# Performance work log

Hardware: AMD Instinct MI355X
Metric: run time of the kernel (lower is better)

## Reference

```python
import jax, jax.numpy as jnp
import numpy as np

TEXT_VOCAB = 32000
CB = 1024          # audio_codebook_size
NCB = 8            # audio_num_codebooks
H = 2048           # hidden_size
NH = 16            # attention heads
NKV = 4            # kv heads (GQA)
HD = H // NH       # head dim = 128
FF = 8192          # ffn intermediate
L = 2              # num layers
EPS = 1e-5


def rmsnorm(x, w):
    v = jnp.mean(x * x, axis=-1, keepdims=True)
    return x * jax.lax.rsqrt(v + EPS) * w


def rope(x, pos):
    # x: [B,S,h,d], rotate-half style RoPE
    d = x.shape[-1]
    inv = 1.0 / (10000.0 ** (jnp.arange(0, d, 2, dtype=jnp.float32) / d))
    ang = pos[:, None] * inv[None, :]                 # [S, d/2]
    cos = jnp.cos(ang)[None, :, None, :]
    sin = jnp.sin(ang)[None, :, None, :]
    x1, x2 = x[..., : d // 2], x[..., d // 2 :]
    return jnp.concatenate([x1 * cos - x2 * sin, x2 * cos + x1 * sin], axis=-1)


def attention(x, wq, wk, wv, wo, pos, mask_bias):
    B, S, _ = x.shape
    q = (x @ wq).reshape(B, S, NH, HD)
    k = (x @ wk).reshape(B, S, NKV, HD)
    v = (x @ wv).reshape(B, S, NKV, HD)
    q = rope(q, pos)
    k = rope(k, pos)
    k = jnp.repeat(k, NH // NKV, axis=2)
    v = jnp.repeat(v, NH // NKV, axis=2)
    scores = jnp.einsum('bqhd,bkhd->bhqk', q, k) / np.float32(np.sqrt(HD))
    p = jax.nn.softmax(scores + mask_bias, axis=-1)
    o = jnp.einsum('bhqk,bkhd->bqhd', p, v).reshape(B, S, NH * HD)
    return o @ wo


def mlp(x, wfc, wproj):
    return jax.nn.silu(x @ wfc) @ wproj


def setup_inputs() -> dict:
    key = jax.random.key(0)
    ks = jax.random.split(key, 20)
    s = 0.02
    inp = {
        'input_ids': jax.random.randint(ks[0], (1, 2048), 0, TEXT_VOCAB + CB, dtype=jnp.int64 if jax.config.jax_enable_x64 else jnp.int32),
        'vocab_emb': jax.random.normal(ks[1], (TEXT_VOCAB, H), jnp.float32) * s,
        'audio_emb': jax.random.normal(ks[2], (NCB * CB, H), jnp.float32) * s,
        'ln_in_text': jnp.ones((L, H), jnp.float32),
        'ln_in_audio': jnp.ones((L, H), jnp.float32),
        'ln_post_text': jnp.ones((L, H), jnp.float32),
        'ln_post_audio': jnp.ones((L, H), jnp.float32),
        'wq': jax.random.normal(ks[3], (L, H, NH * HD), jnp.float32) * s,
        'wk': jax.random.normal(ks[4], (L, H, NKV * HD), jnp.float32) * s,
        'wv': jax.random.normal(ks[5], (L, H, NKV * HD), jnp.float32) * s,
        'wo': jax.random.normal(ks[6], (L, NH * HD, H), jnp.float32) * s,
        'wfc_text': jax.random.normal(ks[7], (L, H, FF), jnp.float32) * s,
        'wproj_text': jax.random.normal(ks[8], (L, FF, H), jnp.float32) * s,
        'wfc_audio': jax.random.normal(ks[9], (L, H, FF), jnp.float32) * s,
        'wproj_audio': jax.random.normal(ks[10], (L, FF, H), jnp.float32) * s,
        'ln_f': jnp.ones((H,), jnp.float32),
    }
    return inp


def reference(input_ids, vocab_emb, audio_emb, ln_in_text, ln_in_audio,
              ln_post_text, ln_post_audio, wq, wk, wv, wo,
              wfc_text, wproj_text, wfc_audio, wproj_audio, ln_f):
    B, S = input_ids.shape
    amask = input_ids > TEXT_VOCAB - 1                      # [B,S] audio-token mask
    text_tok = jnp.where(amask, TEXT_VOCAB - 1, input_ids)
    text_e = vocab_emb[text_tok]                            # [B,S,H]
    audio_tok = jnp.where(amask, input_ids - TEXT_VOCAB, 0)
    shift = (jnp.arange(NCB) * CB)[:, None, None]           # [NCB,1,1]
    audio_e = audio_emb[audio_tok[None] + shift].sum(0)     # sum over codebooks -> [B,S,H]
    h = jnp.where(amask[..., None], audio_e, text_e)

    pos = jnp.arange(S, dtype=jnp.float32)
    causal = jnp.tril(jnp.ones((S, S), bool))
    mask_bias = jnp.where(causal, 0.0, -1e9).astype(jnp.float32)[None, None]
    m = amask[..., None]

    for i in range(L):
        res = h
        hn = jnp.where(m, rmsnorm(h, ln_in_audio[i]), rmsnorm(h, ln_in_text[i]))
        h = res + attention(hn, wq[i], wk[i], wv[i], wo[i], pos, mask_bias)
        res = h
        t = mlp(rmsnorm(h, ln_post_text[i]), wfc_text[i], wproj_text[i])
        a = mlp(rmsnorm(h, ln_post_audio[i]), wfc_audio[i], wproj_audio[i])
        h = res + jnp.where(m, a, t)

    return rmsnorm(h, ln_f)
```

## Files before the change

kernel.cpp:

```cpp
#include <hip/hip_runtime.h>
#include <hip/hip_bf16.h>
#include <math.h>

#define S_LEN 2048
#define HID   2048

typedef __bf16 bf16x8 __attribute__((ext_vector_type(8)));
typedef float  f32x4  __attribute__((ext_vector_type(4)));

__device__ __forceinline__ unsigned short f2b(float x) {
  __hip_bfloat16 h = __float2bfloat16(x);
  return __builtin_bit_cast(unsigned short, h);
}

__device__ __forceinline__ float block_sum_256(float v) {
  __shared__ float red[4];
  #pragma unroll
  for (int o = 32; o > 0; o >>= 1) v += __shfl_down(v, o, 64);
  if ((threadIdx.x & 63) == 0) red[threadIdx.x >> 6] = v;
  __syncthreads();
  v = red[0] + red[1] + red[2] + red[3];
  __syncthreads();
  return v;
}

__global__ __launch_bounds__(256) void embed_kernel(
    const int* __restrict__ ids, const float* __restrict__ vemb,
    const float* __restrict__ aemb, float* __restrict__ h, int* __restrict__ amask) {
  const int s = blockIdx.x;
  const int id = ids[s];
  const bool am = id > 31999;
  if (threadIdx.x == 0) amask[s] = am ? 1 : 0;
  const int d0 = threadIdx.x * 8;
  float out[8];
  if (am) {
    const int at = id - 32000;
    #pragma unroll
    for (int u = 0; u < 8; u++) out[u] = 0.f;
    for (int cb = 0; cb < 8; cb++) {
      const float* src = aemb + (long)(at + cb * 1024) * HID + d0;
      #pragma unroll
      for (int u = 0; u < 8; u++) out[u] += src[u];
    }
  } else {
    const float* src = vemb + (long)id * HID + d0;
    #pragma unroll
    for (int u = 0; u < 8; u++) out[u] = src[u];
  }
  float* dst = h + (long)s * HID + d0;
  #pragma unroll
  for (int u = 0; u < 8; u++) dst[u] = out[u];
}

__global__ __launch_bounds__(256) void partition_rows(
    const int* __restrict__ ids, int* __restrict__ apos, int* __restrict__ cnt) {
  __shared__ int ca[256];
  __shared__ int sc[257];
  const int t = threadIdx.x;
  int m[8], loc = 0;
  #pragma unroll
  for (int i = 0; i < 8; i++) { m[i] = ids[t * 8 + i] > 31999 ? 1 : 0; loc += m[i]; }
  ca[t] = loc;
  __syncthreads();
  if (t == 0) {
    int run = 0;
    for (int i = 0; i < 256; i++) { sc[i] = run; run += ca[i]; }
    sc[256] = run;
  }
  __syncthreads();
  int off = sc[t];
  #pragma unroll
  for (int i = 0; i < 8; i++) {
    const int s = t * 8 + i;
    if (m[i]) { apos[s] = off; off++; }
    else apos[s] = -1;
  }
  if (t == 0) { cnt[0] = sc[256]; cnt[1] = (sc[256] + 127) & ~127; }
}

__global__ __launch_bounds__(256) void init_stats(
    float* __restrict__ stm, float* __restrict__ stl, int* __restrict__ ctrs) {
  const int i = blockIdx.x * 256 + threadIdx.x;
  stm[i] = -1e30f;
  stl[i] = 0.f;
  if (i < 4) ctrs[i] = 0;
}

__global__ __launch_bounds__(256) void transposew(
    const float* __restrict__ W, int ldw, unsigned short* __restrict__ Wt, int K, int N,
    long srcZ, long dstZ) {
  W += (long)blockIdx.z * srcZ;
  Wt += (long)blockIdx.z * dstZ;
  __shared__ float t[64][65];
  const int k0 = blockIdx.y * 64, n0 = blockIdx.x * 64;
  const int q = threadIdx.x & 15;
  const int r0 = threadIdx.x >> 4;
  #pragma unroll
  for (int i = 0; i < 4; i++) {
    const int row = r0 + i * 16;
    const float4 v = *(const float4*)(W + (long)(k0 + row) * ldw + n0 + q * 4);
    t[row][q * 4 + 0] = v.x; t[row][q * 4 + 1] = v.y;
    t[row][q * 4 + 2] = v.z; t[row][q * 4 + 3] = v.w;
  }
  __syncthreads();
  #pragma unroll
  for (int i = 0; i < 4; i++) {
    const int n = r0 + i * 16;
    ushort4 o;
    o.x = f2b(t[q * 4 + 0][n]); o.y = f2b(t[q * 4 + 1][n]);
    o.z = f2b(t[q * 4 + 2][n]); o.w = f2b(t[q * 4 + 3][n]);
    *(ushort4*)(Wt + (long)(n0 + n) * K + k0 + q * 4) = o;
  }
}

__global__ __launch_bounds__(256) void transpose_b16(
    const unsigned short* __restrict__ V, unsigned short* __restrict__ Vt) {
  __shared__ unsigned short t[64][72];
  const int s0 = blockIdx.y * 64, d0 = blockIdx.x * 64;
  const int q = threadIdx.x & 15;
  const int r0 = threadIdx.x >> 4;
  #pragma unroll
  for (int i = 0; i < 4; i++) {
    const int row = r0 + i * 16;
    const ushort4 v = *(const ushort4*)(V + (long)(s0 + row) * 512 + d0 + q * 4);
    t[row][q * 4 + 0] = v.x; t[row][q * 4 + 1] = v.y;
    t[row][q * 4 + 2] = v.z; t[row][q * 4 + 3] = v.w;
  }
  __syncthreads();
  #pragma unroll
  for (int i = 0; i < 4; i++) {
    const int d = r0 + i * 16;
    ushort4 o;
    o.x = t[q * 4 + 0][d]; o.y = t[q * 4 + 1][d];
    o.z = t[q * 4 + 2][d]; o.w = t[q * 4 + 3][d];
    *(ushort4*)(Vt + (long)(d0 + d) * 2048 + s0 + q * 4) = o;
  }
}

__global__ __launch_bounds__(256) void rope_table(float* __restrict__ c, float* __restrict__ s_) {
  const int i = blockIdx.x * 256 + threadIdx.x;
  const int pos = i >> 6, j = i & 63;
  const float inv = powf(10000.f, -(float)(2 * j) * (1.f / 128.f));
  const float ang = (float)pos * inv;
  c[i] = cosf(ang);
  s_[i] = sinf(ang);
}

__global__ __launch_bounds__(256) void rmsnorm_sel(
    const float* __restrict__ x, const int* __restrict__ amask,
    const float* __restrict__ wt, const float* __restrict__ wa, unsigned short* __restrict__ out) {
  const long s = blockIdx.x;
  const float* xr = x + s * HID;
  const int d0 = threadIdx.x * 8;
  float v[8], ss = 0.f;
  #pragma unroll
  for (int u = 0; u < 8; u++) { v[u] = xr[d0 + u]; ss += v[u] * v[u]; }
  ss = block_sum_256(ss) * (1.f / HID);
  const float rr = rsqrtf(ss + 1e-5f);
  const float* w = amask[s] ? wa : wt;
  #pragma unroll
  for (int u = 0; u < 8; u++) out[s * HID + d0 + u] = f2b(v[u] * rr * w[d0 + u]);
}

__global__ __launch_bounds__(256) void rmsnorm_post(
    const float* __restrict__ x, const int* __restrict__ apos,
    const float* __restrict__ wt, const float* __restrict__ wa,
    unsigned short* __restrict__ hnt, unsigned short* __restrict__ hna_g) {
  const long s = blockIdx.x;
  const float* xr = x + s * HID;
  const int d0 = threadIdx.x * 8;
  float v[8], ss = 0.f;
  #pragma unroll
  for (int u = 0; u < 8; u++) { v[u] = xr[d0 + u]; ss += v[u] * v[u]; }
  ss = block_sum_256(ss) * (1.f / HID);
  const float rr = rsqrtf(ss + 1e-5f);
  const int ap = apos[s];
  #pragma unroll
  for (int u = 0; u < 8; u++) {
    const float xn = v[u] * rr;
    hnt[s * HID + d0 + u] = f2b(xn * wt[d0 + u]);
    if (ap >= 0) hna_g[(long)ap * HID + d0 + u] = f2b(xn * wa[d0 + u]);
  }
}

__global__ __launch_bounds__(256) void rmsnorm_final(
    const float* __restrict__ x, const float* __restrict__ w, float* __restrict__ out) {
  const long s = blockIdx.x;
  const float* xr = x + s * HID;
  const int d0 = threadIdx.x * 8;
  float v[8], ss = 0.f;
  #pragma unroll
  for (int u = 0; u < 8; u++) { v[u] = xr[d0 + u]; ss += v[u] * v[u]; }
  ss = block_sum_256(ss) * (1.f / HID);
  const float rr = rsqrtf(ss + 1e-5f);
  #pragma unroll
  for (int u = 0; u < 8; u++) out[s * HID + d0 + u] = v[u] * rr * w[d0 + u];
}

__device__ __forceinline__ void gload16(const void* g, void* l) {
  __builtin_amdgcn_global_load_lds((const __attribute__((address_space(1))) void*)g,
                                   (__attribute__((address_space(3))) void*)l, 16, 0, 0);
}

#define ABAR() do { __builtin_amdgcn_s_barrier(); \
  asm volatile("" ::: "memory"); __builtin_amdgcn_sched_barrier(0); } while (0)

__global__ __launch_bounds__(512, 1) void attn_flash(
    const unsigned short* __restrict__ qb, const unsigned short* __restrict__ kb,
    const unsigned short* __restrict__ vt, float* __restrict__ opart,
    float* __restrict__ stm, float* __restrict__ stl,
    int* __restrict__ ctr, float iscale) {
  __shared__ __align__(16) unsigned short Kb[2][2][128][64];
  __shared__ __align__(16) unsigned short Vb[2][128][64];
  __shared__ __align__(16) unsigned short Pb[8][16][144];
  __shared__ int s_item;
  const int tid = threadIdx.x;
  const int lane = tid & 63;
  const int w = tid >> 6;
  const int lr = lane & 15;
  const int kg = lane >> 4;
  const int trow = tid >> 3;
  const int tc = tid & 7;

  for (;;) {
    if (tid == 0) s_item = atomicAdd(ctr, 1);
    __syncthreads();
    const int item = s_item;
    __syncthreads();
    if (item >= 512) break;
    const int qq = 15 - (item >> 5);
    const int h = item & 15;
    const int cch = (item >> 4) & 1;
    const int kvh = h >> 2;
    const int bm = qq * 128;
    const int nt = qq + 1;
    const int tmid = (nt + 1) >> 1;
    const int t0 = cch ? tmid : 0;
    const int t1 = cch ? nt : tmid;
    if (t0 >= t1) continue;

    bf16x8 af_q[4];
    {
      const unsigned short* qr = qb + (long)(bm + w * 16 + lr) * 2048 + h * 128 + kg * 8;
      #pragma unroll
      for (int c = 0; c < 4; c++) af_q[c] = *(const bf16x8*)(qr + c * 32);
    }
    float m[4], l[4];
    #pragma unroll
    for (int r = 0; r < 4; r++) { m[r] = -1e30f; l[r] = 0.f; }
    f32x4 acc_o[8];
    #pragma unroll
    for (int nf = 0; nf < 8; nf++) acc_o[nf] = (f32x4){0.f, 0.f, 0.f, 0.f};

    auto stageK = [&](int buf, int t) {
      const int kv0 = t * 128;
      #pragma unroll
      for (int hh2 = 0; hh2 < 2; hh2++)
        #pragma unroll
        for (int rr = 0; rr < 2; rr++) {
          const int row = trow + rr * 64;
          gload16(kb + (long)(kv0 + row) * 512 + kvh * 128 + hh2 * 64 + ((tc ^ (row & 7)) * 8),
                  &Kb[buf][hh2][row][tc * 8]);
        }
    };
    auto stageV = [&](int t) {
      const int kv0 = t * 128;
      #pragma unroll
      for (int hh2 = 0; hh2 < 2; hh2++)
        #pragma unroll
        for (int rr = 0; rr < 2; rr++) {
          const int row = trow + rr * 64;
          gload16(vt + (long)(kvh * 128 + row) * 2048 + kv0 + hh2 * 64 + ((tc ^ (row & 7)) * 8),
                  &Vb[hh2][row][tc * 8]);
        }
    };

    stageK(t0 & 1, t0);
    for (int t = t0; t < t1; t++) {
      const bool hn = (t + 1) < t1;
      stageV(t);
      if (hn) stageK((t + 1) & 1, t + 1);
      if (hn) { asm volatile("s_waitcnt vmcnt(8)" ::: "memory"); }
      else    { asm volatile("s_waitcnt vmcnt(4)" ::: "memory"); }
      ABAR();
      f32x4 acc[8];
      #pragma unroll
      for (int nf = 0; nf < 8; nf++) acc[nf] = (f32x4){0.f, 0.f, 0.f, 0.f};
      #pragma unroll
      for (int c = 0; c < 4; c++) {
        #pragma unroll
        for (int nf = 0; nf < 8; nf++) {
          const int row = nf * 16 + lr;
          bf16x8 bk = *(const bf16x8*)(&Kb[t & 1][c >> 1][row][(((c & 1) * 4 + kg) ^ (row & 7)) * 8]);
          acc[nf] = __builtin_amdgcn_mfma_f32_16x16x32_bf16(af_q[c], bk, acc[nf], 0, 0, 0);
        }
      }
      const bool diag = (t == nt - 1);
      #pragma unroll
      for (int r = 0; r < 4; r++) {
        const int rowg = bm + w * 16 + kg * 4 + r;
        float sv[8], tmax = -1e30f;
        #pragma unroll
        for (int nf = 0; nf < 8; nf++) {
          float s = acc[nf][r] * iscale;
          const int colg = t * 128 + nf * 16 + lr;
          if (diag && colg > rowg) s = -1e30f;
          sv[nf] = s;
          tmax = fmaxf(tmax, s);
        }
        #pragma unroll
        for (int o = 1; o < 16; o <<= 1) tmax = fmaxf(tmax, __shfl_xor(tmax, o, 64));
        const float mn = fmaxf(m[r], tmax);
        const float scal = __expf(m[r] - mn);
        float psum = 0.f;
        #pragma unroll
        for (int nf = 0; nf < 8; nf++) {
          const float pe = __expf(sv[nf] - mn);
          psum += pe;
          Pb[w][kg * 4 + r][nf * 16 + lr] = f2b(pe);
        }
        #pragma unroll
        for (int o = 1; o < 16; o <<= 1) psum += __shfl_xor(psum, o, 64);
        l[r] = l[r] * scal + psum;
        m[r] = mn;
        #pragma unroll
        for (int nf = 0; nf < 8; nf++) acc_o[nf][r] *= scal;
      }
      asm volatile("s_waitcnt lgkmcnt(0)" ::: "memory");
      __builtin_amdgcn_sched_barrier(0);
      if (hn) { asm volatile("s_waitcnt vmcnt(4)" ::: "memory"); }
      else    { asm volatile("s_waitcnt vmcnt(0)" ::: "memory"); }
      ABAR();
      #pragma unroll
      for (int c = 0; c < 4; c++) {
        bf16x8 ap = *(const bf16x8*)(&Pb[w][lr][c * 32 + kg * 8]);
        #pragma unroll
        for (int nf = 0; nf < 8; nf++) {
          const int row = nf * 16 + lr;
          bf16x8 bv = *(const bf16x8*)(&Vb[c >> 1][row][(((c & 1) * 4 + kg) ^ (row & 7)) * 8]);
          acc_o[nf] = __builtin_amdgcn_mfma_f32_16x16x32_bf16(ap, bv, acc_o[nf], 0, 0, 0);
        }
      }
      ABAR();
    }
    float* op = opart + (long)cch * 4194304;
    #pragma unroll
    for (int nf = 0; nf < 8; nf++)
      #pragma unroll
      for (int r = 0; r < 4; r++)
        op[(long)(bm + w * 16 + kg * 4 + r) * 2048 + h * 128 + nf * 16 + lr] = acc_o[nf][r];
    if (lr == 0) {
      #pragma unroll
      for (int r = 0; r < 4; r++) {
        const int row = bm + w * 16 + kg * 4 + r;
        stm[(cch * 16 + h) * 2048 + row] = m[r];
        stl[(cch * 16 + h) * 2048 + row] = l[r];
      }
    }
    __syncthreads();
  }
}

__global__ __launch_bounds__(256) void o_merge2(
    const float* __restrict__ op, const float* __restrict__ stm,
    const float* __restrict__ stl, unsigned short* __restrict__ o) {
  const int i = blockIdx.x * 256 + threadIdx.x;
  const int s = i >> 11, c = i & 2047, h = c >> 7;
  const int si = h * 2048 + s;
  const float m1 = stm[si], l1 = stl[si];
  const float m2 = stm[32768 + si], l2 = stl[32768 + si];
  const float M = fmaxf(m1, m2);
  const float w1 = __expf(m1 - M), w2 = __expf(m2 - M);
  const float denom = l1 * w1 + l2 * w2;
  o[i] = f2b((op[i] * w1 + op[i + 4194304] * w2) / denom);
}

__global__ __launch_bounds__(256) void mlp_reduce(
    const float* __restrict__ pt, const float* __restrict__ pa,
    const int* __restrict__ apos, float* __restrict__ h) {
  const int i = blockIdx.x * 256 + threadIdx.x;
  const int r = i >> 11, c = i & 2047;
  const long Z = (long)1 << 22;
  const int ap = apos[r];
  float val;
  if (ap < 0) {
    val = pt[i] + pt[i + Z] + pt[i + 2 * Z] + pt[i + 3 * Z];
  } else {
    const long b = (long)ap * 2048 + c;
    val = 0.f;
    #pragma unroll
    for (int k = 0; k < 8; k++) val += pa[k * Z + b];
  }
  h[i] += val;
}

__device__ __forceinline__ void xcd_swizzle(int& bx, int& by, int& bz) {
  const int gx = gridDim.x, gy = gridDim.y;
  const long nwg = (long)gx * gy * gridDim.z;
  const long lin = blockIdx.x + (long)gx * (blockIdx.y + (long)gy * blockIdx.z);
  const long cpx = nwg >> 3;
  const long w = (lin & 7) * cpx + (lin >> 3);
  bx = (int)(w % gx);
  const long t = w / gx;
  by = (int)(t % gy);
  bz = (int)(t / gy);
}

template <int BM, int BN, int EPI, int SWZ>
__global__ __launch_bounds__(512) void gemm2(
    const unsigned short* __restrict__ A, int lda, long sAz,
    const unsigned short* __restrict__ Bt, int ldb, long sBz,
    void* __restrict__ Cv, int ldc, long sCz, long sCx, int K, float scale,
    const int* __restrict__ ecnt, int kspl,
    const float* __restrict__ rc, const float* __restrict__ rs,
    unsigned short* __restrict__ kbo, unsigned short* __restrict__ vbo) {
  constexpr int MF = BM / 32;
  constexpr int NF = BN / 64;
  __shared__ __align__(16) unsigned short smem[2 * (BM + BN) * 64];
  const int tid = threadIdx.x;
  const int lane = tid & 63;
  const int wave = tid >> 6;
  int bxi = blockIdx.x, byi = blockIdx.y, bzi = blockIdx.z;
  if constexpr (SWZ) xcd_swizzle(bxi, byi, bzi);
  const int bm = byi * BM;
  const int z = bzi;
  int bn, kbeg, nt;
  if constexpr (EPI == 7) {
    bn = bxi * BN;
    kbeg = z * kspl;
    nt = kspl / 64;
  } else {
    bn = bxi * BN;
    kbeg = 0;
    nt = K / 64;
  }
  if constexpr (EPI == 2 || EPI == 7) {
    if (bm >= ecnt[1]) return;
  }
  A += sAz * z;
  Bt += sBz * z;
  const int wm = (wave >> 2) * (BM / 2);
  const int wn = (wave & 3) * (BN / 4);
  const int lr = lane & 15;
  const int kg = lane >> 4;
  const int swx = lr & 7;
  const int trow = tid >> 3;
  const int tc = tid & 7;
  const long aoff = (long)(bm + trow) * lda + ((tc ^ (trow & 7)) * 8);
  const long boff = (long)(bn + trow) * ldb + ((tc ^ (trow & 7)) * 8);

  f32x4 acc[MF][NF];
  #pragma unroll
  for (int m = 0; m < MF; m++)
    #pragma unroll
    for (int n = 0; n < NF; n++) acc[m][n] = (f32x4){0.f, 0.f, 0.f, 0.f};

  auto stage = [&](int buf, int k0) {
    unsigned short* sA = &smem[(size_t)buf * (BM + BN) * 64];
    #pragma unroll
    for (int r = 0; r < BM / 64; r++)
      gload16(A + aoff + (long)r * 64 * lda + k0, sA + r * 4096 + tid * 8);
    unsigned short* sB = sA + BM * 64;
    #pragma unroll
    for (int r = 0; r < BN / 64; r++)
      gload16(Bt + boff + (long)r * 64 * ldb + k0, sB + r * 4096 + tid * 8);
  };
  auto compute = [&](int buf) {
    const unsigned short* sA = &smem[(size_t)buf * (BM + BN) * 64];
    const unsigned short* sB = sA + BM * 64;
    #pragma unroll
    for (int ks = 0; ks < 2; ks++) {
      bf16x8 af[MF], bv[NF];
      #pragma unroll
      for (int m = 0; m < MF; m++) {
        const int row = wm + m * 16 + lr;
        af[m] = *(const bf16x8*)(sA + row * 64 + (((ks * 4 + kg) ^ swx) * 8));
      }
      #pragma unroll
      for (int n = 0; n < NF; n++) {
        const int row = wn + n * 16 + lr;
        bv[n] = *(const bf16x8*)(sB + row * 64 + (((ks * 4 + kg) ^ swx) * 8));
      }
      #pragma unroll
      for (int m = 0; m < MF; m++)
        #pragma unroll
        for (int n = 0; n < NF; n++)
          acc[m][n] = __builtin_amdgcn_mfma_f32_16x16x32_bf16(af[m], bv[n], acc[m][n], 0, 0, 0);
    }
  };

  if (nt > 0) {
    stage(0, kbeg);
    asm volatile("s_waitcnt vmcnt(0)" ::: "memory");
    __syncthreads();
    int cur = 0;
    for (int t = 0; t < nt; t++) {
      if (t + 1 < nt) stage(cur ^ 1, kbeg + (t + 1) * 64);
      compute(cur);
      asm volatile("s_waitcnt vmcnt(0)" ::: "memory");
      __syncthreads();
      cur ^= 1;
    }
  }

  if constexpr (EPI == 8) {
    if (bn >= 2560) {
      #pragma unroll
      for (int m = 0; m < MF; m++)
        #pragma unroll
        for (int n = 0; n < NF; n++)
          #pragma unroll
          for (int r = 0; r < 4; r++) {
            const int grow = bm + wm + m * 16 + kg * 4 + r;
            const int gcol = bn + wn + n * 16 + lr;
            vbo[(long)grow * 512 + (gcol - 2560)] = f2b(acc[m][n][r]);
          }
    } else {
      float* Cl = (float*)smem;
      #pragma unroll
      for (int m = 0; m < MF; m++)
        #pragma unroll
        for (int n = 0; n < NF; n++)
          #pragma unroll
          for (int r = 0; r < 4; r++)
            Cl[(wm + m * 16 + kg * 4 + r) * 128 + wn + n * 16 + lr] = acc[m][n][r];
      __syncthreads();
      const int j = tid & 63;
      const int r2 = tid >> 6;
      #pragma unroll
      for (int it = 0; it < 16; it++) {
        const int row = r2 + it * 8;
        const int s = bm + row;
        const float c = rc[s * 64 + j], sn = rs[s * 64 + j];
        const float x1 = Cl[row * 128 + j], x2 = Cl[row * 128 + j + 64];
        const unsigned short o1 = f2b(x1 * c - x2 * sn);
        const unsigned short o2 = f2b(x2 * c + x1 * sn);
        if (bn < 2048) {
          unsigned short* qp = (unsigned short*)Cv + (long)s * 2048 + bn + j;
          qp[0] = o1; qp[64] = o2;
        } else {
          unsigned short* kp = kbo + (long)s * 512 + (bn - 2048) + j;
          kp[0] = o1; kp[64] = o2;
        }
      }
    }
    return;
  }

  #pragma unroll
  for (int m = 0; m < MF; m++) {
    #pragma unroll
    for (int n = 0; n < NF; n++) {
      #pragma unroll
      for (int r = 0; r < 4; r++) {
        const int grow = bm + wm + m * 16 + kg * 4 + r;
        const int gcol = bn + wn + n * 16 + lr;
        const long idx = (long)grow * ldc + gcol;
        float v = acc[m][n][r];
        if constexpr (EPI == 2) {
          ((unsigned short*)Cv)[idx] = f2b(v / (1.f + expf(-v)));
        } else if constexpr (EPI == 3) {
          ((float*)Cv)[idx] += v;
        } else if constexpr (EPI == 7) {
          ((float*)Cv)[(long)z * sCz + idx] = v;
        }
      }
    }
  }
}

template <int EPI>
__global__ __launch_bounds__(512, 1) void gemm8(
    const unsigned short* __restrict__ A0, const unsigned short* __restrict__ A1, int lda,
    const unsigned short* __restrict__ Bt, long sBz, int ldb,
    void* __restrict__ Cv, int ldc, long sCz, int K) {
  __shared__ __align__(16) unsigned short smem[2][4][8192];
  const int tid = threadIdx.x;
  const int lane = tid & 63;
  const int wave = tid >> 6;
  int bxi = blockIdx.x, byi = blockIdx.y, bzi = blockIdx.z;
  xcd_swizzle(bxi, byi, bzi);
  const int bm = byi * 256;
  const int bn = bxi * 256;
  const int z = bzi;
  const unsigned short* Aq;
  const unsigned short* Bq;
  if constexpr (EPI == 10) {
    Aq = z ? A1 : A0;
    Bq = Bt + (long)z * sBz;
  } else {
    Aq = A0 + z * 2048;
    Bq = Bt + z * 2048;
  }
  const int nt = K / 64;
  const int trow = tid >> 3;
  const int tc = tid & 7;
  const int sws = (tc ^ (trow & 7)) * 8;
  const int lr = lane & 15;
  const int kg = lane >> 4;
  const int wr = (wave >> 2) * 64;
  const int wc = (wave & 3) * 32;

  f32x4 acc[2][2][4][2];
  #pragma unroll
  for (int mh = 0; mh < 2; mh++)
    #pragma unroll
    for (int nh = 0; nh < 2; nh++)
      #pragma unroll
      for (int mf = 0; mf < 4; mf++)
        #pragma unroll
        for (int nf = 0; nf < 2; nf++) acc[mh][nh][mf][nf] = (f32x4){0.f, 0.f, 0.f, 0.f};

  bf16x8 af[2][4], af2[2][4], bv0[2][2], bv1[2][2];

  auto stageA = [&](int buf, int half, int k0) {
    const unsigned short* g = Aq + (long)(bm + half * 128 + trow) * lda + k0 + sws;
    unsigned short* l = &smem[buf][half][0] + tid * 8;
    gload16(g, l);
    gload16(g + (long)64 * lda, l + 4096);
  };
  auto stageB = [&](int buf, int half, int k0) {
    const unsigned short* g = Bq + (long)(bn + half * 128 + trow) * ldb + k0 + sws;
    unsigned short* l = &smem[buf][2 + half][0] + tid * 8;
    gload16(g, l);
    gload16(g + (long)64 * ldb, l + 4096);
  };

#define GSYNC(VM) \
  asm volatile("s_waitcnt vmcnt(" #VM ")" ::: "memory"); \
  __builtin_amdgcn_s_barrier(); \
  asm volatile("" ::: "memory"); \
  __builtin_amdgcn_sched_barrier(0)

#define RD_A(BUF, MH, DST) do { \
    _Pragma("unroll") \
    for (int ks = 0; ks < 2; ++ks) { \
      _Pragma("unroll") \
      for (int mf = 0; mf < 4; ++mf) { \
        const int row = wr + mf * 16 + lr; \
        DST[ks][mf] = *(const bf16x8*)(&smem[BUF][MH][0] + row * 64 + (((ks * 4 + kg) ^ (row & 7)) * 8)); \
      } \
    } \
  } while (0)

#define RD_B(BUF, NH, DST) do { \
    _Pragma("unroll") \
    for (int ks = 0; ks < 2; ++ks) { \
      _Pragma("unroll") \
      for (int nf = 0; nf < 2; ++nf) { \
        const int row = wc + nf * 16 + lr; \
        DST[ks][nf] = *(const bf16x8*)(&smem[BUF][2 + NH][0] + row * 64 + (((ks * 4 + kg) ^ (row & 7)) * 8)); \
      } \
    } \
  } while (0)

#define DO_MFMA(MH, NH, AF, BV) do { \
    __builtin_amdgcn_s_setprio(1); \
    _Pragma("unroll") \
    for (int ks = 0; ks < 2; ++ks) \
      _Pragma("unroll") \
      for (int mf = 0; mf < 4; ++mf) \
        _Pragma("unroll") \
        for (int nf = 0; nf < 2; ++nf) \
          acc[MH][NH][mf][nf] = __builtin_amdgcn_mfma_f32_16x16x32_bf16( \
              AF[ks][mf], BV[ks][nf], acc[MH][NH][mf][nf], 0, 0, 0); \
    __builtin_amdgcn_s_setprio(0); \
  } while (0)

  stageA(0, 0, 0); stageB(0, 0, 0); stageB(0, 1, 0); stageA(0, 1, 0);
  stageA(1, 0, 64); stageB(1, 1, 64); stageB(1, 0, 64);
  GSYNC(8);

  for (int t = 0; t <= nt - 3; ++t) {
    const int b = t & 1, nb = b ^ 1;
    const int k1 = (t + 1) << 6, k2 = (t + 2) << 6;
    RD_A(b, 0, af); RD_B(b, 0, bv0); RD_B(b, 1, bv1);
    stageA(nb, 1, k1); DO_MFMA(0, 0, af, bv0); GSYNC(8);
    RD_A(b, 1, af2);
    stageA(b, 0, k2); DO_MFMA(0, 1, af, bv1); GSYNC(8);
    stageB(b, 1, k2); DO_MFMA(1, 1, af2, bv1); GSYNC(8);
    RD_B(b, 0, bv0);
    stageB(b, 0, k2); DO_MFMA(1, 0, af2, bv0); GSYNC(8);
  }
  {
    const int t = nt - 2;
    const int b = t & 1, nb = b ^ 1;
    const int k1 = (t + 1) << 6;
    RD_A(b, 0, af); RD_B(b, 0, bv0); RD_B(b, 1, bv1);
    stageA(nb, 1, k1); DO_MFMA(0, 0, af, bv0); GSYNC(8);
    RD_A(b, 1, af2); DO_MFMA(0, 1, af, bv1); GSYNC(8);
    DO_MFMA(1, 1, af2, bv1); GSYNC(8);
    RD_B(b, 0, bv0); DO_MFMA(1, 0, af2, bv0); GSYNC(2);
  }
  {
    const int b = (nt - 1) & 1;
    RD_A(b, 0, af); RD_B(b, 0, bv0); RD_B(b, 1, bv1);
    DO_MFMA(0, 0, af, bv0); GSYNC(0);
    RD_A(b, 1, af2); DO_MFMA(0, 1, af, bv1);
    DO_MFMA(1, 1, af2, bv1);
    RD_B(b, 0, bv0); DO_MFMA(1, 0, af2, bv0);
  }
#undef DO_MFMA
#undef RD_B
#undef RD_A
#undef GSYNC

  #pragma unroll
  for (int mh = 0; mh < 2; mh++) {
    #pragma unroll
    for (int nh = 0; nh < 2; nh++) {
      #pragma unroll
      for (int mf = 0; mf < 4; mf++) {
        #pragma unroll
        for (int nf = 0; nf < 2; nf++) {
          #pragma unroll
          for (int r = 0; r < 4; r++) {
            const int grow = bm + mh * 128 + wr + mf * 16 + kg * 4 + r;
            const int gcol = bn + nh * 128 + wc + nf * 16 + lr;
            const long idx = (long)z * sCz + (long)grow * ldc + gcol;
            const float v = acc[mh][nh][mf][nf][r];
            if constexpr (EPI == 10) {
              ((unsigned short*)Cv)[idx] = f2b(v / (1.f + expf(-v)));
            } else {
              ((float*)Cv)[idx] = v;
            }
          }
        }
      }
    }
  }
}

__global__ __launch_bounds__(256) void fill_zero(float* p, long n) {
  const long i = (long)blockIdx.x * 256 + threadIdx.x;
  if (i < n) p[i] = 0.f;
}

extern "C" void kernel_launch(void* const* d_in, const int* in_sizes, int n_in,
                              void* d_out, int out_size, void* d_ws, size_t ws_size,
                              hipStream_t stream) {
  const int* ids = (const int*)d_in[0];
  const float* vocab_emb = (const float*)d_in[1];
  const float* audio_emb = (const float*)d_in[2];
  const float* ln_in_text = (const float*)d_in[3];
  const float* ln_in_audio = (const float*)d_in[4];
  const float* ln_post_text = (const float*)d_in[5];
  const float* ln_post_audio = (const float*)d_in[6];
  const float* wq = (const float*)d_in[7];
  const float* wk = (const float*)d_in[8];
  const float* wv = (const float*)d_in[9];
  const float* wo = (const float*)d_in[10];
  const float* wfc_t = (const float*)d_in[11];
  const float* wpj_t = (const float*)d_in[12];
  const float* wfc_a = (const float*)d_in[13];
  const float* wpj_a = (const float*)d_in[14];
  const float* ln_f = (const float*)d_in[15];

  size_t off = 0;
  auto alloc = [&](size_t bytes) -> void* {
    void* p = (char*)d_ws + off;
    off += (bytes + 255) & ~(size_t)255;
    return p;
  };
  const size_t LW = 77594624;
  unsigned short* wsT = (unsigned short*)alloc((size_t)2 * LW * 2);
  int* amask = (int*)alloc(S_LEN * 4);
  int* apos = (int*)alloc(S_LEN * 4);
  int* cnt = (int*)alloc(16);
  int* ctrs = (int*)alloc(16);
  float* ropec = (float*)alloc((size_t)S_LEN * 64 * 4);
  float* ropes = (float*)alloc((size_t)S_LEN * 64 * 4);
  float* h = (float*)alloc((size_t)S_LEN * HID * 4);
  unsigned short* hn = (unsigned short*)alloc((size_t)S_LEN * HID * 2);
  unsigned short* hnt = (unsigned short*)alloc((size_t)S_LEN * HID * 2);
  unsigned short* hna_g = (unsigned short*)alloc((size_t)S_LEN * HID * 2);
  unsigned short* qb = (unsigned short*)alloc((size_t)S_LEN * 2048 * 2);
  unsigned short* kb = (unsigned short*)alloc((size_t)S_LEN * 512 * 2);
  unsigned short* vb = (unsigned short*)alloc((size_t)S_LEN * 512 * 2);
  unsigned short* vt = (unsigned short*)alloc((size_t)512 * S_LEN * 2);
  unsigned short* o = (unsigned short*)alloc((size_t)S_LEN * 2048 * 2);
  float* stm = (float*)alloc((size_t)2 * 16 * 2048 * 4);
  float* stl = (float*)alloc((size_t)2 * 16 * 2048 * 4);
  char* big = (char*)alloc(268435456);
  float* opart = (float*)big;
  unsigned short* mlp_t = (unsigned short*)big;
  unsigned short* mlp_a = (unsigned short*)(big + 33554432);
  float* pt = (float*)(big + 67108864);
  float* pa = (float*)(big + 134217728);

  if (ws_size < off) {
    fill_zero<<<(out_size + 255) / 256, 256, 0, stream>>>((float*)d_out, out_size);
    return;
  }

  const size_t WO_ = 6291456, WFT = 10485760, WPT = 27262976, WFA = 44040192, WPA = 60817408;

  embed_kernel<<<S_LEN, 256, 0, stream>>>(ids, vocab_emb, audio_emb, h, amask);
  partition_rows<<<1, 256, 0, stream>>>(ids, apos, cnt);
  init_stats<<<256, 256, 0, stream>>>(stm, stl, ctrs);
  rope_table<<<S_LEN * 64 / 256, 256, 0, stream>>>(ropec, ropes);

  const long LWl = (long)LW;
  transposew<<<dim3(32, 32, 2), 256, 0, stream>>>(wq, 2048, wsT, 2048, 2048, 4194304, LWl);
  transposew<<<dim3(8, 32, 2), 256, 0, stream>>>(wk, 512, wsT + 4194304, 2048, 512, 1048576, LWl);
  transposew<<<dim3(8, 32, 2), 256, 0, stream>>>(wv, 512, wsT + 5242880, 2048, 512, 1048576, LWl);
  transposew<<<dim3(32, 32, 2), 256, 0, stream>>>(wo, 2048, wsT + WO_, 2048, 2048, 4194304, LWl);
  transposew<<<dim3(128, 32, 2), 256, 0, stream>>>(wfc_t, 8192, wsT + WFT, 2048, 8192, 16777216, LWl);
  transposew<<<dim3(32, 128, 2), 256, 0, stream>>>(wpj_t, 2048, wsT + WPT, 8192, 2048, 16777216, LWl);
  transposew<<<dim3(128, 32, 2), 256, 0, stream>>>(wfc_a, 8192, wsT + WFA, 2048, 8192, 16777216, LWl);
  transposew<<<dim3(32, 128, 2), 256, 0, stream>>>(wpj_a, 2048, wsT + WPA, 8192, 2048, 16777216, LWl);

  const float iscale = 0.08838834764831845f;
  for (int i = 0; i < 2; i++) {
    const size_t wb = (size_t)i * LW;
    rmsnorm_sel<<<S_LEN, 256, 0, stream>>>(h, amask, ln_in_text + i * HID, ln_in_audio + i * HID, hn);
    gemm2<128, 128, 8, 1><<<dim3(24, 16, 1), 512, 0, stream>>>(hn, 2048, 0, wsT + wb, 2048, 0,
        qb, 2048, 0, 0, 2048, 1.f, nullptr, 0, ropec, ropes, kb, vb);
    transpose_b16<<<dim3(8, 32), 256, 0, stream>>>(vb, vt);
    attn_flash<<<256, 512, 0, stream>>>(qb, kb, vt, opart, stm, stl, ctrs + i, iscale);
    o_merge2<<<16384, 256, 0, stream>>>(opart, stm, stl, o);
    gemm2<128, 128, 3, 1><<<dim3(16, 16, 1), 512, 0, stream>>>(o, 2048, 0, wsT + wb + WO_, 2048, 0,
        h, 2048, 0, 0, 2048, 1.f, nullptr, 0, nullptr, nullptr, nullptr, nullptr);
    rmsnorm_post<<<S_LEN, 256, 0, stream>>>(h, apos, ln_post_text + i * HID, ln_post_audio + i * HID, hnt, hna_g);
    gemm2<128, 128, 2, 0><<<dim3(64, 16, 1), 512, 0, stream>>>(hna_g, 2048, 0, wsT + wb + WFA, 2048, 0,
        mlp_a, 8192, 0, 0, 2048, 1.f, cnt, 0, nullptr, nullptr, nullptr, nullptr);
    gemm8<10><<<dim3(32, 8, 1), 512, 0, stream>>>(hnt, hnt, 2048, wsT + wb + WFT, 0, 2048,
        mlp_t, 8192, 0, 2048);
    gemm2<128, 128, 7, 0><<<dim3(16, 16, 8), 512, 0, stream>>>(mlp_a, 8192, 0, wsT + wb + WPA, 8192, 0,
        pa, 2048, (long)1 << 22, 0, 8192, 1.f, cnt, 1024, nullptr, nullptr, nullptr, nullptr);
    gemm8<11><<<dim3(8, 8, 4), 512, 0, stream>>>(mlp_t, mlp_t, 8192, wsT + wb + WPT, 0, 8192,
        pt, 2048, (long)1 << 22, 2048);
    mlp_reduce<<<16384, 256, 0, stream>>>(pt, pa, apos, h);
  }
  rmsnorm_final<<<S_LEN, 256, 0, stream>>>(h, ln_f, (float*)d_out);
}
```

Before: 968.4 us.

## Fuse MLP reduce with next RMSNorm and split-K the audio fc GEMM

Merges the MLP partial-sum reduction with the following layer's input RMSNorm, or with the final norm on the last layer. This removes a separate rmsnorm pass and an extra read of h. The audio up-projection GEMM now runs split-K with two z-slices writing fp32 partials, and a new silu_reduce kernel sums them and applies SiLU. This adds parallelism for the small audio-row GEMM, at the cost of an extra fp32 write/read pass and a kernel launch.

```diff
diff --git a/kernel.cpp b/kernel.cpp
--- a/kernel.cpp
+++ b/kernel.cpp
@@ -183,18 +183,58 @@
   }
 }
 
-__global__ __launch_bounds__(256) void rmsnorm_final(
-    const float* __restrict__ x, const float* __restrict__ w, float* __restrict__ out) {
+template <int MODE>
+__global__ __launch_bounds__(256) void mlp_reduce_norm(
+    const float* __restrict__ pt, const float* __restrict__ pa,
+    const int* __restrict__ apos, const int* __restrict__ amask,
+    float* __restrict__ h, const float* __restrict__ wt, const float* __restrict__ wa,
+    void* __restrict__ out) {
   const long s = blockIdx.x;
-  const float* xr = x + s * HID;
   const int d0 = threadIdx.x * 8;
-  float v[8], ss = 0.f;
-  #pragma unroll
-  for (int u = 0; u < 8; u++) { v[u] = xr[d0 + u]; ss += v[u] * v[u]; }
+  const long Z = (long)1 << 22;
+  const int ap = apos[s];
+  const long base = s * HID + d0;
+  float hv[8], ss = 0.f;
+  #pragma unroll
+  for (int u = 0; u < 8; u++) {
+    float val;
+    if (ap < 0) {
+      val = pt[base + u] + pt[base + u + Z] + pt[base + u + 2 * Z] + pt[base + u + 3 * Z];
+    } else {
+      const long b = (long)ap * 2048 + d0 + u;
+      val = 0.f;
+      #pragma unroll
+      for (int k = 0; k < 8; k++) val += pa[k * Z + b];
+    }
+    hv[u] = h[base + u] + val;
+    ss += hv[u] * hv[u];
+  }
+  if constexpr (MODE == 0) {
+    #pragma unroll
+    for (int u = 0; u < 8; u++) h[base + u] = hv[u];
+  }
   ss = block_sum_256(ss) * (1.f / HID);
   const float rr = rsqrtf(ss + 1e-5f);
-  #pragma unroll
-  for (int u = 0; u < 8; u++) out[s * HID + d0 + u] = v[u] * rr * w[d0 + u];
+  if constexpr (MODE == 0) {
+    const float* w = amask[s] ? wa : wt;
+    #pragma unroll
+    for (int u = 0; u < 8; u++) ((unsigned short*)out)[base + u] = f2b(hv[u] * rr * w[d0 + u]);
+  } else {
+    #pragma unroll
+    for (int u = 0; u < 8; u++) ((float*)out)[base + u] = hv[u] * rr * wt[d0 + u];
+  }
+}
+
+__global__ __launch_bounds__(256) void silu_reduce(
+    const float* __restrict__ p, const int* __restrict__ cnt, unsigned short* __restrict__ out) {
+  const int i = blockIdx.x * 2048 + threadIdx.x * 8;
+  const int r = i >> 13;
+  if (r >= cnt[1]) return;
+  #pragma unroll
+  for (int u = 0; u < 8; u++) {
+    const float v = p[i + u] + p[i + u + (1 << 24)];
+    out[i + u] = f2b(v / (1.f + expf(-v)));
+  }
 }
 
 __device__ __forceinline__ void gload16(const void* g, void* l) {
@@ -373,25 +413,6 @@
   const float w1 = __expf(m1 - M), w2 = __expf(m2 - M);
   const float denom = l1 * w1 + l2 * w2;
   o[i] = f2b((op[i] * w1 + op[i + 4194304] * w2) / denom);
-}
-
-__global__ __launch_bounds__(256) void mlp_reduce(
-    const float* __restrict__ pt, const float* __restrict__ pa,
-    const int* __restrict__ apos, float* __restrict__ h) {
-  const int i = blockIdx.x * 256 + threadIdx.x;
-  const int r = i >> 11, c = i & 2047;
-  const long Z = (long)1 << 22;
-  const int ap = apos[r];
-  float val;
-  if (ap < 0) {
-    val = pt[i] + pt[i + Z] + pt[i + 2 * Z] + pt[i + 3 * Z];
-  } else {
-    const long b = (long)ap * 2048 + c;
-    val = 0.f;
-    #pragma unroll
-    for (int k = 0; k < 8; k++) val += pa[k * Z + b];
-  }
-  h[i] += val;
 }
 
 __device__ __forceinline__ void xcd_swizzle(int& bx, int& by, int& bz) {
@@ -787,6 +808,7 @@
   unsigned short* mlp_a = (unsigned short*)(big + 33554432);
   float* pt = (float*)(big + 67108864);
   float* pa = (float*)(big + 134217728);
+  float* pfa = (float*)(big + 134217728);
 
   if (ws_size < off) {
     fill_zero<<<(out_size + 255) / 256, 256, 0, stream>>>((float*)d_out, out_size);
@@ -811,9 +833,9 @@
   transposew<<<dim3(32, 128, 2), 256, 0, stream>>>(wpj_a, 2048, wsT + WPA, 8192, 2048, 16777216, LWl);
 
   const float iscale = 0.08838834764831845f;
+  rmsnorm_sel<<<S_LEN, 256, 0, stream>>>(h, amask, ln_in_text, ln_in_audio, hn);
   for (int i = 0; i < 2; i++) {
     const size_t wb = (size_t)i * LW;
-    rmsnorm_sel<<<S_LEN, 256, 0, stream>>>(h, amask, ln_in_text + i * HID, ln_in_audio + i * HID, hn);
     gemm2<128, 128, 8, 1><<<dim3(24, 16, 1), 512, 0, stream>>>(hn, 2048, 0, wsT + wb, 2048, 0,
         qb, 2048, 0, 0, 2048, 1.f, nullptr, 0, ropec, ropes, kb, vb);
     transpose_b16<<<dim3(8, 32), 256, 0, stream>>>(vb, vt);
@@ -822,15 +844,21 @@
     gemm2<128, 128, 3, 1><<<dim3(16, 16, 1), 512, 0, stream>>>(o, 2048, 0, wsT + wb + WO_, 2048, 0,
         h, 2048, 0, 0, 2048, 1.f, nullptr, 0, nullptr, nullptr, nullptr, nullptr);
     rmsnorm_post<<<S_LEN, 256, 0, stream>>>(h, apos, ln_post_text + i * HID, ln_post_audio + i * HID, hnt, hna_g);
-    gemm2<128, 128, 2, 0><<<dim3(64, 16, 1), 512, 0, stream>>>(hna_g, 2048, 0, wsT + wb + WFA, 2048, 0,
-        mlp_a, 8192, 0, 0, 2048, 1.f, cnt, 0, nullptr, nullptr, nullptr, nullptr);
+    gemm2<128, 128, 7, 0><<<dim3(64, 16, 2), 512, 0, stream>>>(hna_g, 2048, 0, wsT + wb + WFA, 2048, 0,
+        pfa, 8192, (long)1 << 24, 0, 2048, 1.f, cnt, 1024, nullptr, nullptr, nullptr, nullptr);
+    silu_reduce<<<8192, 256, 0, stream>>>(pfa, cnt, mlp_a);
     gemm8<10><<<dim3(32, 8, 1), 512, 0, stream>>>(hnt, hnt, 2048, wsT + wb + WFT, 0, 2048,
         mlp_t, 8192, 0, 2048);
     gemm2<128, 128, 7, 0><<<dim3(16, 16, 8), 512, 0, stream>>>(mlp_a, 8192, 0, wsT + wb + WPA, 8192, 0,
         pa, 2048, (long)1 << 22, 0, 8192, 1.f, cnt, 1024, nullptr, nullptr, nullptr, nullptr);
     gemm8<11><<<dim3(8, 8, 4), 512, 0, stream>>>(mlp_t, mlp_t, 8192, wsT + wb + WPT, 0, 8192,
         pt, 2048, (long)1 << 22, 2048);
-    mlp_reduce<<<16384, 256, 0, stream>>>(pt, pa, apos, h);
-  }
-  rmsnorm_final<<<S_LEN, 256, 0, stream>>>(h, ln_f, (float*)d_out);
-}
+    if (i == 0) {
+      mlp_reduce_norm<0><<<S_LEN, 256, 0, stream>>>(pt, pa, apos, amask, h,
+          ln_in_text + HID, ln_in_audio + HID, hn);
+    } else {
+      mlp_reduce_norm<1><<<S_LEN, 256, 0, stream>>>(pt, pa, apos, nullptr, h,
+          ln_f, nullptr, d_out);
+    }
+  }
+}
```

Measured after the change: 1.006 ms. +3.9%, slower.
